# Optimization experiments

Measured on AMD Instinct MI355X. Metric: run time of the kernel, lower is better.

Reference implementation:

```python
import jax, jax.numpy as jnp
import numpy as np

B, N, E, HD, L, LH, NC = 256, 96, 1024, 300, 2, 600, 7

def prelu(x, a):
    return jnp.where(x >= 0, x, a * x)

def setup_inputs():
    key = jax.random.key(0)
    ks = jax.random.split(key, 16)
    s = 0.02
    r = lambda i, shp: jax.random.normal(ks[i], shp, jnp.float32) * s
    z = lambda shp: jnp.zeros(shp, jnp.float32)
    GD = HD * (L + 1)
    inp = {}
    inp["features"] = jax.random.normal(ks[0], (B, N, E), jnp.float32)
    inp["s_mask"] = jax.random.randint(ks[1], (B, N, N), 0, 2, jnp.int32)
    inp["entro"] = jax.random.uniform(ks[2], (B, N), dtype=jnp.float32)
    inp["alpha"] = 0.5
    inp["threshold"] = 0.25
    inp["fc1_w"] = r(3, (HD, E)); inp["fc1_b"] = z((HD,))
    inp["gat_w"] = r(4, (L, 2 * HD)); inp["gat_b"] = z((L,))
    inp["wr0"] = r(5, (L, HD, HD)); inp["wr1"] = r(6, (L, HD, HD))
    inp["enhance_w"] = r(7, (E, E)); inp["enhance_b"] = z((E,))
    inp["prelu_a"] = jnp.array(0.25, jnp.float32)
    inp["lstm_w_ih"] = r(8, (4 * LH, E + GD)); inp["lstm_w_hh"] = r(9, (4 * LH, LH))
    inp["lstm_b_ih"] = z((4 * LH,)); inp["lstm_b_hh"] = z((4 * LH,))
    inp["mlp_w0"] = r(10, (HD, LH)); inp["mlp_b0"] = z((HD,)); inp["mlp_a0"] = jnp.array(0.25, jnp.float32)
    inp["mlp_w1"] = r(11, (HD, HD)); inp["mlp_b1"] = z((HD,)); inp["mlp_a1"] = jnp.array(0.25, jnp.float32)
    inp["out_w"] = r(12, (NC, HD)); inp["out_b"] = z((NC,))
    return inp

def reference(features, s_mask, entro, alpha, threshold, fc1_w, fc1_b, gat_w, gat_b, wr0, wr1, enhance_w, enhance_b, prelu_a, lstm_w_ih, lstm_w_hh, lstm_b_ih, lstm_b_hh, mlp_w0, mlp_b0, mlp_a0, mlp_w1, mlp_b1, mlp_a1, out_w, out_b):
    # context_filter: cosine similarity + entropy edge filtering -> binary adjacency (B,N,N)
    f = features / (jnp.linalg.norm(features, axis=-1, keepdims=True) + 1e-8)
    sim = jnp.einsum("bid,bjd->bij", f, f)
    comb = alpha * entro[:, None, :] + (1.0 - alpha) * sim
    adj = comb > threshold
    H0 = prelu(features @ fc1_w.T + fc1_b, prelu_a)
    sm = s_mask.astype(features.dtype)
    Hs = [H0]
    for l in range(L):
        Hl = Hs[-1]
        wq, wk = gat_w[l, :HD], gat_w[l, HD:]
        # fused GAT over all target nodes i: score[b,i,j] = wq.H[b,i] + wk.H[b,j] + b
        scores = (Hl @ wq)[:, :, None] + (Hl @ wk)[:, None, :] + gat_b[l]
        scores = jnp.where(adj, scores, -1e9)
        attn = jax.nn.softmax(scores, axis=-1)
        V0 = Hl @ wr0[l].T  # relation-0 transform
        V1 = Hl @ wr1[l].T  # relation-1 transform
        M = jnp.einsum("bij,bjd->bid", attn * sm, V0) + jnp.einsum("bij,bjd->bid", attn * (1.0 - sm), V1)
        Hs.append(M)
    Hcat = jnp.concatenate(Hs, axis=2)  # (B, N, HD*(L+1))
    feat = prelu(features @ enhance_w.T + enhance_b, prelu_a)
    seq = jnp.concatenate([feat, Hcat], axis=-1)
    zin = seq @ lstm_w_ih.T + lstm_b_ih + lstm_b_hh  # (B, N, 4*LH), input projection hoisted out of scan
    def step(carry, zt):
        h, c = carry
        g = zt + h @ lstm_w_hh.T
        i, fg, gg, o = jnp.split(g, 4, axis=-1)
        c = jax.nn.sigmoid(fg) * c + jax.nn.sigmoid(i) * jnp.tanh(gg)
        h = jax.nn.sigmoid(o) * jnp.tanh(c)
        return (h, c), h
    h0 = jnp.zeros((features.shape[0], LH), features.dtype)
    _, hs = jax.lax.scan(step, (h0, h0), jnp.swapaxes(zin, 0, 1))
    Hl = jnp.swapaxes(hs, 0, 1)  # (B, N, LH)
    x = prelu(Hl @ mlp_w0.T + mlp_b0, mlp_a0)
    x = prelu(x @ mlp_w1.T + mlp_b1, mlp_a1)
    return x @ out_w.T + out_b  # (B, N, NC)
```

## Files before the change

kernel.cpp:

```cpp
#include <hip/hip_runtime.h>
#include <cstdint>
#include <cstddef>

#define Bdim 256
#define Ndim 96
#define Edim 1024
#define HDdim 300
#define Ldim 2
#define LHdim 600
#define NCdim 7
#define GDdim 900
#define ROWS (Bdim*Ndim)
#define HSLICE 155648

typedef unsigned short u16;
typedef unsigned int   u32;
typedef float f32x4 __attribute__((ext_vector_type(4)));
typedef short bf16x8 __attribute__((ext_vector_type(8)));
typedef unsigned short u16x4 __attribute__((ext_vector_type(4)));

#define IDP 0x7FFFFFFF, 1, 30, 0, 0

__device__ inline u16 f2bf(float x) {
    u32 u = __builtin_bit_cast(u32, x);
    u32 r = (u + 0x7fffu + ((u >> 16) & 1u)) >> 16;
    return (u16)r;
}
__device__ inline float bf2f(u16 h) {
    u32 u = ((u32)h) << 16;
    return __builtin_bit_cast(float, u);
}

template<int OUT, int ACT>
__global__ __launch_bounds__(256) void gemm_bf16(
    const u16* __restrict__ Ah, int lda,
    const u16* __restrict__ Wh, int ldw,
    float* __restrict__ C, u16* __restrict__ Ch, int ldc,
    int M, int Nd, int K,
    const float* __restrict__ bias, const float* __restrict__ aptr)
{
    __shared__ u16 At[4][1024];
    __shared__ u16 Wt[4][1024];
    const int tid  = threadIdx.x;
    const int ny  = gridDim.y;
    const int nwg = gridDim.x * ny;
    const int lin = blockIdx.y * gridDim.x + blockIdx.x;
    const int q = nwg >> 3, r8 = nwg & 7;
    const int xcd = lin & 7, off = lin >> 3;
    const int swz = (xcd < r8) ? xcd * (q + 1) + off
                               : r8 * (q + 1) + (xcd - r8) * q + off;
    const int bm   = (swz / ny) * 128;
    const int bn   = (swz % ny) * 128;
    const int wv   = tid >> 6;
    const int lane = tid & 63;
    const int wr   = (wv >> 1) * 64;
    const int wc   = (wv & 1) * 64;
    const int l15  = lane & 15;
    const int kseg = lane >> 4;

    f32x4 acc[4][4];
    #pragma unroll
    for (int i = 0; i < 4; ++i)
        #pragma unroll
        for (int j = 0; j < 4; ++j) acc[i][j] = (f32x4){0.f,0.f,0.f,0.f};

    const int srow = tid & 127;
    const bool isA = (tid < 128);
    const int gr   = isA ? (bm + srow) : (bn + srow);
    const int glim = isA ? M : 0x7FFFFFFF;
    const u16* pbase = (isA ? Ah : Wh) + (size_t)gr * (isA ? lda : ldw);
    u16* dst = isA ? &At[0][0] : &Wt[0][0];

    for (int k0 = 0; k0 < K; k0 += 32) {
        __syncthreads();
        {
            const bool ok = (gr < glim);
            #pragma unroll
            for (int s = 0; s < 4; ++s) {
                bf16x8 v = {0,0,0,0,0,0,0,0};
                if (ok) v = *(const bf16x8*)(pbase + k0 + s * 8);
                *(bf16x8*)(dst + s * 1024 + srow * 8) = v;
            }
        }
        __syncthreads();
        bf16x8 a[4], b[4];
        #pragma unroll
        for (int f = 0; f < 4; ++f) {
            int ar = wr + f * 16 + l15;
            int br = wc + f * 16 + l15;
            a[f] = *(const bf16x8*)&At[kseg][ar * 8];
            b[f] = *(const bf16x8*)&Wt[kseg][br * 8];
        }
        #pragma unroll
        for (int i = 0; i < 4; ++i)
            #pragma unroll
            for (int j = 0; j < 4; ++j)
                acc[i][j] = __builtin_amdgcn_mfma_f32_16x16x32_bf16(a[i], b[j], acc[i][j], 0, 0, 0);
    }

    const float av = (ACT == 1) ? *aptr : 0.f;
    const int r4 = (lane >> 4) * 4;
    #pragma unroll
    for (int j = 0; j < 4; ++j) {
        int col = bn + wc + j * 16 + l15;
        if (col >= Nd) continue;
        float bv = bias ? bias[col] : 0.f;
        #pragma unroll
        for (int i = 0; i < 4; ++i) {
            #pragma unroll
            for (int rr = 0; rr < 4; ++rr) {
                int row = bm + wr + i * 16 + r4 + rr;
                if (row >= M) continue;
                float v = acc[i][j][rr] + bv;
                if (ACT == 1) v = (v >= 0.f) ? v : av * v;
                if (OUT == 0) {
                    C[(size_t)row * ldc + col] = v;
                } else {
                    Ch[(size_t)row * ldc + col] = f2bf(v);
                }
            }
        }
    }
}

__global__ __launch_bounds__(256) void split_rows8(
    const float* __restrict__ src, int srcld,
    int pmask, int pmul1, int pshift, int pmul2, int padd,
    u16* __restrict__ dstH, int dstld,
    int wcols, int validK, int validRows)
{
    const int r = blockIdx.y * 4 + (threadIdx.x >> 6);
    const int c = (blockIdx.x * 64 + (threadIdx.x & 63)) * 8;
    if (c >= wcols) return;
    const int sr = (r & pmask) * pmul1 + (r >> pshift) * pmul2 + padd;
    const float* s = src + (size_t)sr * srcld;
    const bool rok = (r < validRows);
    float v[8];
    if (rok && c + 8 <= validK) {
        *(float4*)&v[0] = *(const float4*)(s + c);
        *(float4*)&v[4] = *(const float4*)(s + c + 4);
    } else {
        #pragma unroll
        for (int u = 0; u < 8; ++u) v[u] = (rok && c + u < validK) ? s[c + u] : 0.f;
    }
    bf16x8 H8;
    #pragma unroll
    for (int u = 0; u < 8; ++u) H8[u] = (short)f2bf(v[u]);
    *(bf16x8*)(dstH + (size_t)r * dstld + c) = H8;
}

__global__ __launch_bounds__(256) void bias_perm(
    const float* __restrict__ bih, const float* __restrict__ bhh, float* __restrict__ dst)
{
    int n = blockIdx.x * 256 + threadIdx.x;
    if (n >= 4 * LHdim) return;
    int o = (n & 3) * LHdim + (n >> 2);
    dst[n] = bih[o] + bhh[o];
}

__global__ __launch_bounds__(256) void wr_cat(
    const float* __restrict__ wr0, const float* __restrict__ wr1, float* __restrict__ dst)
{
    int c = blockIdx.x * 256 + threadIdx.x;
    if (c >= HDdim) return;
    int lr = blockIdx.y;
    int l = lr / (2 * HDdim), r = lr % (2 * HDdim);
    const float* src = (r < HDdim)
        ? wr0 + ((size_t)l * HDdim + r) * HDdim
        : wr1 + ((size_t)l * HDdim + (r - HDdim)) * HDdim;
    dst[(size_t)lr * HDdim + c] = src[c];
}

__global__ __launch_bounds__(256) void zero_range(float* __restrict__ p, int n)
{
    int i = blockIdx.x * 256 + threadIdx.x;
    if (i < n) p[i] = 0.f;
}

__global__ __launch_bounds__(256) void norm_kernel(const float* __restrict__ f, float* __restrict__ invn)
{
    int row  = blockIdx.x * 4 + (threadIdx.x >> 6);
    int lane = threadIdx.x & 63;
    const float* fr = f + (size_t)row * Edim;
    float ss = 0.f;
    for (int t = lane; t < Edim; t += 64) { float v = fr[t]; ss = fmaf(v, v, ss); }
    #pragma unroll
    for (int o = 32; o > 0; o >>= 1) ss += __shfl_down(ss, o);
    if (lane == 0) invn[row] = 1.f / (sqrtf(ss) + 1e-8f);
}

__global__ __launch_bounds__(256) void simadj_kernel(
    const float* __restrict__ f, const float* __restrict__ invn,
    const float* __restrict__ entro, const float* __restrict__ alphap,
    const float* __restrict__ thrp, uint8_t* __restrict__ adj)
{
    int b = blockIdx.x;
    __shared__ float S[16][100];
    int tid = threadIdx.x;
    int i0 = (tid >> 4) * 6, j0 = (tid & 15) * 6;
    float acc[6][6];
    #pragma unroll
    for (int i = 0; i < 6; ++i)
        #pragma unroll
        for (int j = 0; j < 6; ++j) acc[i][j] = 0.f;
    const float* fb = f + (size_t)b * Ndim * Edim;

    for (int k0 = 0; k0 < Edim; k0 += 16) {
        __syncthreads();
        #pragma unroll
        for (int r = 0; r < 6; ++r) {
            int n = (tid >> 4) + r * 16;
            S[tid & 15][n] = fb[(size_t)n * Edim + k0 + (tid & 15)];
        }
        __syncthreads();
        #pragma unroll
        for (int kk = 0; kk < 16; ++kk) {
            float a[6], bb[6];
            #pragma unroll
            for (int u = 0; u < 6; ++u) a[u] = S[kk][i0 + u];
            #pragma unroll
            for (int u = 0; u < 6; ++u) bb[u] = S[kk][j0 + u];
            #pragma unroll
            for (int i = 0; i < 6; ++i)
                #pragma unroll
                for (int j = 0; j < 6; ++j)
                    acc[i][j] = fmaf(a[i], bb[j], acc[i][j]);
        }
    }

    float alpha = *alphap, thr = *thrp;
    float onem = 1.f - alpha;
    #pragma unroll
    for (int i = 0; i < 6; ++i) {
        int ii = i0 + i;
        float inv_i = invn[b * Ndim + ii];
        #pragma unroll
        for (int j = 0; j < 6; ++j) {
            int jj = j0 + j;
            float simv = acc[i][j] * inv_i * invn[b * Ndim + jj];
            float comb = alpha * entro[b * Ndim + jj] + onem * simv;
            adj[((size_t)b * Ndim + ii) * Ndim + jj] = (comb > thr) ? 1 : 0;
        }
    }
}

__global__ __launch_bounds__(256) void k_kernel(
    const float* __restrict__ Hsrc, const float* __restrict__ wk,
    float* __restrict__ k)
{
    int row  = blockIdx.x * 4 + (threadIdx.x >> 6);
    int lane = threadIdx.x & 63;
    const float* h = Hsrc + (size_t)row * GDdim;
    float sk = 0.f;
    for (int t = lane; t < HDdim; t += 64) sk = fmaf(h[t], wk[t], sk);
    #pragma unroll
    for (int o = 32; o > 0; o >>= 1) sk += __shfl_down(sk, o);
    if (lane == 0) k[row] = sk;
}

__global__ __launch_bounds__(256) void gat_fused(
    const float* __restrict__ kbuf, const uint8_t* __restrict__ adj,
    const int* __restrict__ smask,
    const float* __restrict__ V,
    float* __restrict__ Mout)
{
    __shared__ u16 P0[96][100];
    __shared__ u16 P1[96][100];
    __shared__ u16 Vs0[96][96];
    __shared__ u16 Vs1[96][96];
    __shared__ float ek[96];
    __shared__ float rden[96];
    __shared__ float red[256];
    const int b = blockIdx.x;
    const int half = blockIdx.y;
    const int tid = threadIdx.x;

    float kj = (tid < Ndim) ? kbuf[tid * Bdim + b] : -1e30f;
    red[tid] = kj;
    __syncthreads();
    #pragma unroll
    for (int s = 128; s > 0; s >>= 1) {
        if (tid < s) red[tid] = fmaxf(red[tid], red[tid + s]);
        __syncthreads();
    }
    float kmax = red[0];
    if (tid < Ndim) ek[tid] = expf(kj - kmax);
    __syncthreads();
    if (tid < Ndim) {
        const uint8_t* ar = adj + ((size_t)b * Ndim + tid) * Ndim;
        float s = 0.f;
        for (int j = 0; j < Ndim; ++j) if (ar[j]) s += ek[j];
        rden[tid] = 1.f / s;
    }
    __syncthreads();
    for (int idx = tid; idx < Ndim * Ndim; idx += 256) {
        int i = idx / Ndim, j = idx - i * Ndim;
        float a = adj[((size_t)b * Ndim + i) * Ndim + j] ? ek[j] * rden[i] : 0.f;
        int s = smask[((size_t)b * Ndim + i) * Ndim + j];
        P0[i][j] = s ? f2bf(a) : (u16)0;
        P1[i][j] = s ? (u16)0 : f2bf(a);
    }
    __syncthreads();

    const int ti = tid >> 4, td = tid & 15;
    const int i0 = ti * 6, dbase = td * 6;
    for (int p = 2 * half; p < 2 * half + 2; ++p) {
        const int d0 = p * 96;
        const int dw = (p == 3) ? (HDdim - 288) : 96;
        for (int idx = tid; idx < 96 * 24; idx += 256) {
            int j = idx / 24, q4 = (idx - j * 24) * 4;
            if (q4 < dw) {
                size_t g = ((size_t)(j * Bdim + b)) * (2 * HDdim) + d0 + q4;
                float4 a = *(const float4*)(V + g);
                float4 c = *(const float4*)(V + g + HDdim);
                u16x4 ua = { f2bf(a.x), f2bf(a.y), f2bf(a.z), f2bf(a.w) };
                u16x4 uc = { f2bf(c.x), f2bf(c.y), f2bf(c.z), f2bf(c.w) };
                *(u16x4*)&Vs0[j][q4] = ua;
                *(u16x4*)&Vs1[j][q4] = uc;
            }
        }
        __syncthreads();
        float acc[6][6];
        #pragma unroll
        for (int ii = 0; ii < 6; ++ii)
            #pragma unroll
            for (int dd = 0; dd < 6; ++dd) acc[ii][dd] = 0.f;
        for (int j = 0; j < Ndim; j += 2) {
            float paj[6], pajn[6], pbj[6], pbjn[6];
            #pragma unroll
            for (int ii = 0; ii < 6; ++ii) {
                u32 w0 = *(const u32*)&P0[i0 + ii][j];
                u32 w1 = *(const u32*)&P1[i0 + ii][j];
                paj[ii]  = __builtin_bit_cast(float, w0 << 16);
                pajn[ii] = __builtin_bit_cast(float, w0 & 0xffff0000u);
                pbj[ii]  = __builtin_bit_cast(float, w1 << 16);
                pbjn[ii] = __builtin_bit_cast(float, w1 & 0xffff0000u);
            }
            float v0a[6], v0b[6], v1a[6], v1b[6];
            #pragma unroll
            for (int dd = 0; dd < 3; ++dd) {
                u32 wa = *(const u32*)&Vs0[j][dbase + 2 * dd];
                u32 wb = *(const u32*)&Vs0[j + 1][dbase + 2 * dd];
                u32 wc2 = *(const u32*)&Vs1[j][dbase + 2 * dd];
                u32 wd = *(const u32*)&Vs1[j + 1][dbase + 2 * dd];
                v0a[2*dd]   = __builtin_bit_cast(float, wa << 16);
                v0a[2*dd+1] = __builtin_bit_cast(float, wa & 0xffff0000u);
                v0b[2*dd]   = __builtin_bit_cast(float, wb << 16);
                v0b[2*dd+1] = __builtin_bit_cast(float, wb & 0xffff0000u);
                v1a[2*dd]   = __builtin_bit_cast(float, wc2 << 16);
                v1a[2*dd+1] = __builtin_bit_cast(float, wc2 & 0xffff0000u);
                v1b[2*dd]   = __builtin_bit_cast(float, wd << 16);
                v1b[2*dd+1] = __builtin_bit_cast(float, wd & 0xffff0000u);
            }
            #pragma unroll
            for (int ii = 0; ii < 6; ++ii)
                #pragma unroll
                for (int dd = 0; dd < 6; ++dd) {
                    acc[ii][dd] += paj[ii]  * v0a[dd] + pbj[ii]  * v1a[dd]
                                 + pajn[ii] * v0b[dd] + pbjn[ii] * v1b[dd];
                }
        }
        __syncthreads();
        #pragma unroll
        for (int ii = 0; ii < 6; ++ii) {
            #pragma unroll
            for (int dd = 0; dd < 6; ++dd) {
                int d = dbase + dd;
                if (d < dw)
                    Mout[((size_t)((i0 + ii) * Bdim + b)) * GDdim + d0 + d] = acc[ii][dd];
            }
        }
    }
}

__global__ __launch_bounds__(256) void lstm_bf16(
    const u16* __restrict__ hH,
    const float* __restrict__ cin,
    const u16* __restrict__ WH,
    const float* __restrict__ zt,
    u16* __restrict__ hHo,
    float* __restrict__ cout)
{
    __shared__ u16 As[2][4][256];
    __shared__ u16 Ws[2][4][512];
    __shared__ __align__(16) float gates[32][68];
    const int tid = threadIdx.x;
    const int bm = blockIdx.x * 32;
    const int bn = blockIdx.y * 64;
    const int wv = tid >> 6;
    const int lane = tid & 63;
    const int l15 = lane & 15;
    const int kseg = lane >> 4;
    const float4 fz = make_float4(0.f, 0.f, 0.f, 0.f);

    const int prow0 = tid >> 4,        pui0 = tid & 15;
    const int prow1 = (tid + 256) >> 4, pui1 = tid & 15;
    const int pn0 = bn + pui0 * 4,  pn1 = bn + pui1 * 4;
    const int pu0 = pn0 >> 2,       pu1 = pn1 >> 2;
    const bool ok0 = (pu0 < LHdim), ok1 = (pu1 < LHdim);
    const int bb0 = bm + prow0,     bb1 = bm + prow1;
    float4 z0 = ok0 ? *(const float4*)(zt + (size_t)bb0 * (4 * LHdim) + pn0) : fz;
    float4 z1 = ok1 ? *(const float4*)(zt + (size_t)bb1 * (4 * LHdim) + pn1) : fz;
    float ci0 = ok0 ? cin[bb0 * LHdim + pu0] : 0.f;
    float ci1 = ok1 ? cin[bb1 * LHdim + pu1] : 0.f;

    const int av = tid & 127;
    const int arow = av >> 2, akc = av & 3;
    const u16* asrc = hH + (size_t)(bm + arow) * 608 + akc * 8;
    const int aoff = akc * 256 + arow * 8;
    const bool doA = (tid < 128);
    const int wrow = tid >> 2, wkc = tid & 3;
    const u16* wsrc = WH + (size_t)(bn + wrow) * 608 + wkc * 8;
    const int woff2 = wrow * 8;

    f32x4 acc[2];
    acc[0] = (f32x4){0.f,0.f,0.f,0.f};
    acc[1] = (f32x4){0.f,0.f,0.f,0.f};

    bf16x8 ra = *(const bf16x8*)(asrc);
    bf16x8 rw = *(const bf16x8*)(wsrc);

    #pragma unroll
    for (int kc = 0; kc < 19; ++kc) {
        const int buf = kc & 1;
        if (doA) *(bf16x8*)(&As[buf][0][0] + aoff) = ra;
        *(bf16x8*)(&Ws[buf][wkc][woff2]) = rw;
        if (kc + 1 < 19) {
            ra = *(const bf16x8*)(asrc + (kc + 1) * 32);
            rw = *(const bf16x8*)(wsrc + (kc + 1) * 32);
        }
        __syncthreads();
        bf16x8 a0, a1, b;
        a0 = *(const bf16x8*)&As[buf][kseg][(l15) * 8];
        a1 = *(const bf16x8*)&As[buf][kseg][(16 + l15) * 8];
        b  = *(const bf16x8*)&Ws[buf][kseg][(wv * 16 + l15) * 8];
        acc[0] = __builtin_amdgcn_mfma_f32_16x16x32_bf16(a0, b, acc[0], 0, 0, 0);
        acc[1] = __builtin_amdgcn_mfma_f32_16x16x32_bf16(a1, b, acc[1], 0, 0, 0);
    }

    const int r4 = (lane >> 4) * 4;
    __syncthreads();
    #pragma unroll
    for (int i = 0; i < 2; ++i)
        #pragma unroll
        for (int rr = 0; rr < 4; ++rr)
            gates[i * 16 + r4 + rr][wv * 16 + l15] = acc[i][rr];
    __syncthreads();

    if (ok0) {
        float4 g = *(const float4*)&gates[prow0][pui0 * 4];
        float gi = g.x + z0.x;
        float gf = g.y + z0.y;
        float gg = g.z + z0.z;
        float go = g.w + z0.w;
        float si = 1.f / (1.f + expf(-gi));
        float sf = 1.f / (1.f + expf(-gf));
        float so = 1.f / (1.f + expf(-go));
        float cn = sf * ci0 + si * tanhf(gg);
        float hn = so * tanhf(cn);
        cout[bb0 * LHdim + pu0] = cn;
        hHo[(size_t)bb0 * 608 + pu0] = f2bf(hn);
    }
    if (ok1) {
        float4 g = *(const float4*)&gates[prow1][pui1 * 4];
        float gi = g.x + z1.x;
        float gf = g.y + z1.y;
        float gg = g.z + z1.z;
        float go = g.w + z1.w;
        float si = 1.f / (1.f + expf(-gi));
        float sf = 1.f / (1.f + expf(-gf));
        float so = 1.f / (1.f + expf(-go));
        float cn = sf * ci1 + si * tanhf(gg);
        float hn = so * tanhf(cn);
        cout[bb1 * LHdim + pu1] = cn;
        hHo[(size_t)bb1 * 608 + pu1] = f2bf(hn);
    }
}

__global__ __launch_bounds__(256) void out_kernel(
    const float* __restrict__ x, int ldx, const float* __restrict__ ow,
    const float* __restrict__ ob, float* __restrict__ out)
{
    int r    = blockIdx.x * 4 + (threadIdx.x >> 6);
    int lane = threadIdx.x & 63;
    const float* xr = x + (size_t)r * ldx;
    float acc[NCdim];
    #pragma unroll
    for (int n = 0; n < NCdim; ++n) acc[n] = 0.f;
    for (int t = lane; t < HDdim; t += 64) {
        float xv = xr[t];
        #pragma unroll
        for (int n = 0; n < NCdim; ++n) acc[n] = fmaf(xv, ow[n * HDdim + t], acc[n]);
    }
    #pragma unroll
    for (int o = 32; o > 0; o >>= 1)
        #pragma unroll
        for (int n = 0; n < NCdim; ++n) acc[n] += __shfl_down(acc[n], o);
    if (lane == 0) {
        int b = r & 255, nn = r >> 8;
        #pragma unroll
        for (int n = 0; n < NCdim; ++n) out[((size_t)b * Ndim + nn) * NCdim + n] = acc[n] + ob[n];
    }
}

extern "C" void kernel_launch(void* const* d_in, const int* in_sizes, int n_in,
                              void* d_out, int out_size, void* d_ws, size_t ws_size,
                              hipStream_t stream)
{
    const float*  features  = (const float*)d_in[0];
    const int*    s_mask    = (const int*)  d_in[1];
    const float*  entro     = (const float*)d_in[2];
    const float*  alpha     = (const float*)d_in[3];
    const float*  threshold = (const float*)d_in[4];
    const float*  fc1_w     = (const float*)d_in[5];
    const float*  fc1_b     = (const float*)d_in[6];
    const float*  gat_w     = (const float*)d_in[7];
    const float*  gat_b     = (const float*)d_in[8];
    const float*  wr0       = (const float*)d_in[9];
    const float*  wr1       = (const float*)d_in[10];
    const float*  enhance_w = (const float*)d_in[11];
    const float*  enhance_b = (const float*)d_in[12];
    const float*  prelu_a   = (const float*)d_in[13];
    const float*  lstm_w_ih = (const float*)d_in[14];
    const float*  lstm_w_hh = (const float*)d_in[15];
    const float*  lstm_b_ih = (const float*)d_in[16];
    const float*  lstm_b_hh = (const float*)d_in[17];
    const float*  mlp_w0    = (const float*)d_in[18];
    const float*  mlp_b0    = (const float*)d_in[19];
    const float*  mlp_a0    = (const float*)d_in[20];
    const float*  mlp_w1    = (const float*)d_in[21];
    const float*  mlp_b1    = (const float*)d_in[22];
    const float*  mlp_a1    = (const float*)d_in[23];
    const float*  out_w     = (const float*)d_in[24];
    const float*  out_b     = (const float*)d_in[25];
    float* out = (float*)d_out;
    char* ws = (char*)d_ws;
    (void)gat_b;

    uint8_t* adj   = (uint8_t*)(ws + 0);
    float*   invn  = (float*)(ws + 2359296);
    float*   kbuf  = (float*)(ws + 2457600);
    float*   biasP = (float*)(ws + 2555904);
    float*   c0    = (float*)(ws + 2566144);
    float*   c1    = (float*)(ws + 3180544);
    u16*     WhhPH = (u16*)(ws + 3794944);
    u16*     WihPH = (u16*)(ws + 6752256);
    u16*     EwH   = (u16*)(ws + 16246784);
    u16*     Fc1H  = (u16*)(ws + 18343936);
    float*   Wr2f  = (float*)(ws + 19130368);
    u16*     Wr2H  = (u16*)(ws + 20570368);
    u16*     Wm0H  = (u16*)(ws + 21389568);
    u16*     Wm1H  = (u16*)(ws + 21856512);
    u16*     FfH   = (u16*)(ws + 22102272);
    float*   Hcat  = (float*)(ws + 72433920);
    u16*     HsH   = (u16*)(ws + 160907520);
    float*   V      = (float*)(ws + 176636160);
    u16*     HlstmH = (u16*)(ws + 176636160);
    u16*     x1H   = (u16*)Hcat;
    float*   x2    = (float*)(ws + 72433920 + 31457280);

    const size_t fixedNeed = 235618560ull;
    const size_t perT = 3457024ull;
    int T;
    if      (ws_size >= fixedNeed + 96ull * perT) T = 96;
    else if (ws_size >= fixedNeed + 48ull * perT) T = 48;
    else if (ws_size >= fixedNeed + 32ull * perT) T = 32;
    else if (ws_size >= fixedNeed + 16ull * perT) T = 16;
    else if (ws_size >= fixedNeed +  8ull * perT) T = 8;
    else return;
    char* cr = ws + fixedNeed;
    float* zin  = (float*)cr;
    u16*   seqH = (u16*)(cr + (size_t)T * 2457600);

    norm_kernel<<<ROWS / 4, 256, 0, stream>>>(features, invn);
    simadj_kernel<<<Bdim, 256, 0, stream>>>(features, invn, entro, alpha, threshold, adj);

    split_rows8<<<dim3(2, ROWS / 4), 256, 0, stream>>>(
        features, Edim, 255, Ndim, 8, 1, 0, FfH, Edim, Edim, Edim, ROWS);
    split_rows8<<<dim3(2, 96), 256, 0, stream>>>(
        fc1_w, Edim, IDP, Fc1H, Edim, Edim, Edim, HDdim);
    split_rows8<<<dim3(2, 256), 256, 0, stream>>>(
        enhance_w, Edim, IDP, EwH, Edim, Edim, Edim, Edim);
    split_rows8<<<dim3(4, 608), 256, 0, stream>>>(
        lstm_w_ih, Edim + GDdim, 3, LHdim, 2, 1, 0, WihPH, 1952, 1952, 1924, 2400);
    split_rows8<<<dim3(2, 608), 256, 0, stream>>>(
        lstm_w_hh, LHdim, 3, LHdim, 2, 1, 0, WhhPH, 608, 608, LHdim, 2400);
    split_rows8<<<dim3(2, 96), 256, 0, stream>>>(
        mlp_w0, LHdim, IDP, Wm0H, 608, 608, LHdim, HDdim);
    split_rows8<<<dim3(1, 96), 256, 0, stream>>>(
        mlp_w1, HDdim, IDP, Wm1H, 320, 320, HDdim, HDdim);
    wr_cat<<<dim3(2, 2 * Ldim * HDdim), 256, 0, stream>>>(wr0, wr1, Wr2f);
    for (int l = 0; l < Ldim; ++l)
        split_rows8<<<dim3(1, 160), 256, 0, stream>>>(
            Wr2f + (size_t)l * 2 * HDdim * HDdim, HDdim, IDP,
            Wr2H + (size_t)l * 640 * 320, 320, 320, HDdim, 2 * HDdim);
    bias_perm<<<10, 256, 0, stream>>>(lstm_b_ih, lstm_b_hh, biasP);
    zero_range<<<1200, 256, 0, stream>>>(c0, 307200);

    gemm_bf16<0,1><<<dim3(ROWS/128, 3), 256, 0, stream>>>(
        FfH, Edim, Fc1H, Edim,
        Hcat, nullptr, GDdim, ROWS, HDdim, Edim, fc1_b, prelu_a);

    for (int l = 0; l < Ldim; ++l) {
        const float* Hsrc = Hcat + l * HDdim;
        k_kernel<<<ROWS / 4, 256, 0, stream>>>(Hsrc, gat_w + l * 2 * HDdim + HDdim, kbuf);
        split_rows8<<<dim3(1, ROWS / 4), 256, 0, stream>>>(
            Hsrc, GDdim, IDP, HsH, 320, 320, HDdim, ROWS);
        gemm_bf16<0,0><<<dim3(ROWS/128, 5), 256, 0, stream>>>(
            HsH, 320, Wr2H + (size_t)l * 640 * 320, 320,
            V, nullptr, 2 * HDdim, ROWS, 2 * HDdim, 320, nullptr, nullptr);
        gat_fused<<<dim3(Bdim, 2), 256, 0, stream>>>(
            kbuf, adj, s_mask, V, Hcat + (l + 1) * HDdim);
    }

    zero_range<<<29489, 256, 0, stream>>>((float*)HlstmH, 7548928);

    int cur = 0;
    float* cb_[2] = {c0, c1};
    for (int t0 = 0; t0 < Ndim; t0 += T) {
        int Mc = T * Bdim;
        gemm_bf16<1,1><<<dim3(Mc/128, 8), 256, 0, stream>>>(
            FfH + (size_t)t0 * Bdim * Edim, Edim, EwH, Edim,
            nullptr, seqH, 1952, Mc, Edim, Edim, enhance_b, prelu_a);
        split_rows8<<<dim3(2, Mc / 4), 256, 0, stream>>>(
            Hcat, GDdim, 0x7FFFFFFF, 1, 30, 0, t0 * Bdim,
            seqH + 1024, 1952, 928, GDdim, Mc);
        gemm_bf16<0,0><<<dim3(Mc/128, 19), 256, 0, stream>>>(
            seqH, 1952, WihPH, 1952,
            zin, nullptr, 4 * LHdim, Mc, 4 * LHdim, 1952, biasP, nullptr);
        for (int tl = 0; tl < T; ++tl) {
            const int g = t0 + tl;
            lstm_bf16<<<dim3(8, 38), 256, 0, stream>>>(
                HlstmH + (size_t)g * HSLICE, cb_[cur], WhhPH,
                zin + (size_t)tl * Bdim * 4 * LHdim,
                HlstmH + (size_t)(g + 1) * HSLICE, cb_[cur ^ 1]);
            cur ^= 1;
        }
    }

    zero_range<<<15360, 256, 0, stream>>>((float*)x1H, 3932160);
    gemm_bf16<1,1><<<dim3(ROWS/128, 3), 256, 0, stream>>>(
        HlstmH + HSLICE, 608, Wm0H, 608,
        nullptr, x1H, 320, ROWS, HDdim, 608, mlp_b0, mlp_a0);
    gemm_bf16<0,1><<<dim3(ROWS/128, 3), 256, 0, stream>>>(
        x1H, 320, Wm1H, 320,
        x2, nullptr, 304, ROWS, HDdim, 320, mlp_b1, mlp_a1);
    out_kernel<<<ROWS / 4, 256, 0, stream>>>(x2, 304, out_w, out_b, out);
}
```

Baseline: 2.628 ms.

## Double-buffer LDS tiles with register prefetch in bf16 GEMM

The bf16 MFMA GEMM now keeps two LDS buffers and loads the next K-chunk from global memory into registers while the current chunk is computed. This drops one of the two barriers per iteration and hides global load latency behind MFMA work. The row bound check on A is also removed, so it relies on M being a multiple of the tile height. It doubles LDS use per block, which may lower occupancy.

```diff
diff --git a/kernel.cpp b/kernel.cpp
--- a/kernel.cpp
+++ b/kernel.cpp
@@ -39,8 +39,8 @@
     int M, int Nd, int K,
     const float* __restrict__ bias, const float* __restrict__ aptr)
 {
-    __shared__ u16 At[4][1024];
-    __shared__ u16 Wt[4][1024];
+    __shared__ u16 At[2][4][1024];
+    __shared__ u16 Wt[2][4][1024];
     const int tid  = threadIdx.x;
     const int ny  = gridDim.y;
     const int nwg = gridDim.x * ny;
@@ -67,29 +67,33 @@
     const int srow = tid & 127;
     const bool isA = (tid < 128);
     const int gr   = isA ? (bm + srow) : (bn + srow);
-    const int glim = isA ? M : 0x7FFFFFFF;
     const u16* pbase = (isA ? Ah : Wh) + (size_t)gr * (isA ? lda : ldw);
-    u16* dst = isA ? &At[0][0] : &Wt[0][0];
-
-    for (int k0 = 0; k0 < K; k0 += 32) {
+    u16* dst = isA ? &At[0][0][0] : &Wt[0][0][0];
+    const int soff = srow * 8;
+
+    bf16x8 rv[4];
+    #pragma unroll
+    for (int s = 0; s < 4; ++s) rv[s] = *(const bf16x8*)(pbase + s * 8);
+
+    const int nk = K >> 5;
+    for (int kc = 0; kc < nk; ++kc) {
+        const int bufo = (kc & 1) << 12;
+        #pragma unroll
+        for (int s = 0; s < 4; ++s)
+            *(bf16x8*)(dst + bufo + s * 1024 + soff) = rv[s];
+        if (kc + 1 < nk) {
+            const u16* p = pbase + (kc + 1) * 32;
+            #pragma unroll
+            for (int s = 0; s < 4; ++s) rv[s] = *(const bf16x8*)(p + s * 8);
+        }
         __syncthreads();
-        {
-            const bool ok = (gr < glim);
-            #pragma unroll
-            for (int s = 0; s < 4; ++s) {
-                bf16x8 v = {0,0,0,0,0,0,0,0};
-                if (ok) v = *(const bf16x8*)(pbase + k0 + s * 8);
-                *(bf16x8*)(dst + s * 1024 + srow * 8) = v;
-            }
-        }
-        __syncthreads();
+        const u16* Ab = &At[0][0][0] + bufo + kseg * 1024;
+        const u16* Wb = &Wt[0][0][0] + bufo + kseg * 1024;
         bf16x8 a[4], b[4];
         #pragma unroll
         for (int f = 0; f < 4; ++f) {
-            int ar = wr + f * 16 + l15;
-            int br = wc + f * 16 + l15;
-            a[f] = *(const bf16x8*)&At[kseg][ar * 8];
-            b[f] = *(const bf16x8*)&Wt[kseg][br * 8];
+            a[f] = *(const bf16x8*)(Ab + (wr + f * 16 + l15) * 8);
+            b[f] = *(const bf16x8*)(Wb + (wc + f * 16 + l15) * 8);
         }
         #pragma unroll
         for (int i = 0; i < 4; ++i)
```

Result: faster. 2.437 ms (-7.3%).
